# Optimization experiments

Hardware: AMD Instinct MI355X
Metric: run time of the kernel (lower is better)

The kernel has to match this reference:

```python
import jax, jax.numpy as jnp
import numpy as np

NINP, NHID, NPROJ, NLAYER = 240, 1024, 512, 3


def setup_inputs() -> dict:
    key = jax.random.key(0)
    keys = jax.random.split(key, 1 + NLAYER * 6)
    inp = {"x": jax.random.normal(keys[0], (500, 32, NINP), dtype=jnp.float32)}
    kit = iter(keys[1:])
    for l in range(NLAYER):
        nin = NINP if l == 0 else NPROJ
        s = 1.0 / np.sqrt(nin + NPROJ)
        inp[f"W{l}"] = jax.random.uniform(next(kit), (4 * NHID, nin + NPROJ), minval=-s, maxval=s, dtype=jnp.float32)
        inp[f"b{l}"] = jax.random.uniform(next(kit), (4 * NHID,), minval=-s, maxval=s, dtype=jnp.float32)
        sp = 1.0 / np.sqrt(NHID)
        inp[f"P{l}"] = jax.random.uniform(next(kit), (NPROJ, NHID), minval=-sp, maxval=sp, dtype=jnp.float32)
        inp[f"pi{l}"] = jax.random.normal(next(kit), (NHID,), dtype=jnp.float32) * 0.1
        inp[f"pf{l}"] = jax.random.normal(next(kit), (NHID,), dtype=jnp.float32) * 0.1
        inp[f"po{l}"] = jax.random.normal(next(kit), (NHID,), dtype=jnp.float32) * 0.1
    return inp


def _lstmp_layer(x, W, b, P, pi, pf, po):
    # x: [T, B, nin]; returns [T, B, nproj]
    T, B, _ = x.shape
    h0 = jnp.zeros((B, NPROJ), x.dtype)
    c0 = jnp.zeros((B, NHID), x.dtype)

    def step(carry, xt):
        hx, cx = carry
        gates = jnp.concatenate([xt, hx], axis=1) @ W.T + b  # [B, 4*nhid]
        c_in, i_g, f_g, o_g = jnp.split(gates, 4, axis=1)
        i_g = jax.nn.sigmoid(i_g + pi * cx)
        f_g = jax.nn.sigmoid(f_g + pf * cx)
        cy = jnp.clip(f_g * cx + i_g * jnp.tanh(c_in), -50.0, 50.0)
        o_g = jax.nn.sigmoid(o_g + po * cy)
        hy = (o_g * jnp.tanh(cy)) @ P.T  # [B, nproj]
        return (hy, cy), hy

    _, ys = jax.lax.scan(step, (h0, c0), x)
    return ys


def reference(x, W0, b0, P0, pi0, pf0, po0, W1, b1, P1, pi1, pf1, po1, W2, b2, P2, pi2, pf2, po2):
    y = _lstmp_layer(x, W0, b0, P0, pi0, pf0, po0)
    y = _lstmp_layer(y, W1, b1, P1, pi1, pf1, po1)
    y = _lstmp_layer(y, W2, b2, P2, pi2, pf2, po2)
    return y
```

## Files before the change

### kernel.cpp

```cpp
#include <hip/hip_runtime.h>


typedef short s16x4 __attribute__((ext_vector_type(4)));
typedef short s16x8 __attribute__((ext_vector_type(8)));
typedef float f32x4 __attribute__((ext_vector_type(4)));

#define MFMA16(a,b,c) __builtin_amdgcn_mfma_f32_16x16x32_bf16((a),(b),(c),0,0,0)

__device__ __forceinline__ unsigned short f2bf(float f) {
  unsigned int u = __builtin_bit_cast(unsigned int, f);
  u += 0x7FFFu + ((u >> 16) & 1u);
  return (unsigned short)(u >> 16);
}
__device__ __forceinline__ float bf2f(unsigned short h) {
  unsigned int u = ((unsigned int)h) << 16;
  return __builtin_bit_cast(float, u);
}
__device__ __forceinline__ float fsig(float x)  { return __fdividef(1.0f, 1.0f + __expf(-x)); }
__device__ __forceinline__ float ftanh(float x) { return 1.0f - __fdividef(2.0f, 1.0f + __expf(2.0f * x)); }

__device__ __forceinline__ s16x8 cload(const unsigned short* p) {
  unsigned long long a = __hip_atomic_load((unsigned long long*)p,       __ATOMIC_RELAXED, __HIP_MEMORY_SCOPE_AGENT);
  unsigned long long b = __hip_atomic_load((unsigned long long*)(p + 4), __ATOMIC_RELAXED, __HIP_MEMORY_SCOPE_AGENT);
  s16x4 x = __builtin_bit_cast(s16x4, a);
  s16x4 y = __builtin_bit_cast(s16x4, b);
  s16x8 r = {x[0], x[1], x[2], x[3], y[0], y[1], y[2], y[3]};
  return r;
}
__device__ __forceinline__ void cstore1(unsigned short* p, unsigned short v) {
  __hip_atomic_store(p, v, __ATOMIC_RELAXED, __HIP_MEMORY_SCOPE_AGENT);
}

__device__ __forceinline__ void gbar(unsigned int* bar, unsigned int* rel, unsigned int seq) {
  __syncthreads();
  asm volatile("" ::: "memory");
  if (blockIdx.x == 0) {
    const int tid = threadIdx.x;
    if (tid > 0 && tid < 192) {
      while (__hip_atomic_load(&bar[tid * 16], __ATOMIC_RELAXED, __HIP_MEMORY_SCOPE_AGENT) != seq) {
        __builtin_amdgcn_s_sleep(1);
      }
    }
    __syncthreads();
    if (tid == 0) {
      __hip_atomic_store(rel, seq, __ATOMIC_RELAXED, __HIP_MEMORY_SCOPE_AGENT);
    }
  } else {
    if (threadIdx.x == 0) {
      __hip_atomic_store(&bar[blockIdx.x * 16], seq, __ATOMIC_RELAXED, __HIP_MEMORY_SCOPE_AGENT);
      while (__hip_atomic_load(rel, __ATOMIC_RELAXED, __HIP_MEMORY_SCOPE_AGENT) != seq) {
        __builtin_amdgcn_s_sleep(1);
      }
    }
    __syncthreads();
  }
  asm volatile("" ::: "memory");
}

__global__ __launch_bounds__(512, 2) void lstmp_persist(
    const float* __restrict__ x,
    const float* __restrict__ W0, const float* __restrict__ b0, const float* __restrict__ P0,
    const float* __restrict__ pi0, const float* __restrict__ pf0, const float* __restrict__ po0,
    const float* __restrict__ W1, const float* __restrict__ b1, const float* __restrict__ P1,
    const float* __restrict__ pi1, const float* __restrict__ pf1, const float* __restrict__ po1,
    const float* __restrict__ W2, const float* __restrict__ b2, const float* __restrict__ P2,
    const float* __restrict__ pi2, const float* __restrict__ pf2, const float* __restrict__ po2,
    float* __restrict__ out, unsigned char* __restrict__ ws)
{
  const int tid  = threadIdx.x;
  const int bid  = blockIdx.x;
  const int lane = tid & 63;
  const int wv   = tid >> 6;
  const int quad8 = (lane >> 4) * 8;
  const int nrow  = lane & 15;

  unsigned int* bar   = (unsigned int*)ws;
  unsigned int* rel   = bar + 4096;
  unsigned int* mflag = rel + 16;
  unsigned short* xhi = (unsigned short*)(ws + 20480);
  unsigned short* xlo  = xhi  + 4096000;
  unsigned short* hhi  = xlo  + 4096000;
  unsigned short* hlo  = hhi  + 98304;
  unsigned short* mhi  = hlo  + 98304;
  unsigned short* mlo  = mhi  + 98304;

  const float* Wsrc[3] = {W0, W1, W2};
  const float* Psrc[3] = {P0, P1, P2};
  const float* Bsrc[3] = {b0, b1, b2};
  const float* PIs[3]  = {pi0, pi1, pi2};
  const float* PFs[3]  = {pf0, pf1, pf2};
  const float* POs[3]  = {po0, po1, po2};

  __shared__ float exch[8][4][512];
  __shared__ float c_lds[512];
  __shared__ float lds_pad[4096];
  ((volatile float*)lds_pad)[tid & 4095] = 0.0f;

  const unsigned int NT = 192u * 512u;
  const unsigned int gtid = (unsigned int)bid * 512u + (unsigned int)tid;

  const int lA  = bid >> 6;
  const int utA = bid & 63;
  const int ptC = (bid & 63) >> 1;
  const int mtC = bid & 1;

  const int nkbinA  = (lA == 0) ? 8   : 16;
  const int kinpadA = (lA == 0) ? 256 : 512;
  const int kbwA    = (lA == 0) ? 3   : 4;
  const int kwA     = (lA == 0) ? 752 : 1024;
  const int ninA    = (lA == 0) ? 240 : 512;
  const int kb0     = wv * kbwA;

  for (unsigned int i = gtid; i < 4096000u; i += NT) {
    unsigned int k = i & 255u, tb = i >> 8;
    float v = (k < 240u) ? x[tb * 240u + k] : 0.0f;
    unsigned short h = f2bf(v);
    xhi[i] = h; xlo[i] = f2bf(v - bf2f(h));
  }
  for (unsigned int i = gtid; i < 98304u; i += NT) { hhi[i] = 0; hlo[i] = 0; }
  c_lds[tid] = 0.0f;

  s16x8 wgh[4][4], wgl[4][4];
  {
    const float* Wl = Wsrc[lA];
    #pragma unroll
    for (int j = 0; j < 4; ++j) {
      if (j < kbwA) {
        const int kbase = (kb0 + j) * 32 + quad8;
        #pragma unroll
        for (int g = 0; g < 4; ++g) {
          const size_t r = (size_t)((g * 64 + utA) * 16 + nrow);
          #pragma unroll
          for (int jj = 0; jj < 8; ++jj) {
            const int k = kbase + jj;
            float v;
            if (k < kinpadA) v = (lA == 0 && k >= 240) ? 0.0f : Wl[r * kwA + k];
            else             v = Wl[r * kwA + (k - kinpadA + ninA)];
            unsigned short h = f2bf(v);
            wgh[j][g][jj] = (short)h;
            wgl[j][g][jj] = (short)f2bf(v - bf2f(h));
          }
        }
      } else {
        #pragma unroll
        for (int g = 0; g < 4; ++g) { wgh[j][g] = (s16x8)0; wgl[j][g] = (s16x8)0; }
      }
    }
  }
  s16x8 wph[4], wpl[4];
  {
    const float* Pl = Psrc[lA];
    const size_t prow = (size_t)(ptC * 16 + nrow);
    #pragma unroll
    for (int j = 0; j < 4; ++j) {
      const int kbase = (wv * 4 + j) * 32 + quad8;
      #pragma unroll
      for (int jj = 0; jj < 8; ++jj) {
        float v = Pl[prow * 1024u + (size_t)(kbase + jj)];
        unsigned short h = f2bf(v);
        wph[j][jj] = (short)h;
        wpl[j][jj] = (short)f2bf(v - bf2f(h));
      }
    }
  }
  const int uc = utA * 16 + (tid & 15);
  const float rbc = Bsrc[lA][uc];
  const float rbi = Bsrc[lA][1024 + uc];
  const float rbf = Bsrc[lA][2048 + uc];
  const float rbo = Bsrc[lA][3072 + uc];
  const float rpi = PIs[lA][uc];
  const float rpf = PFs[lA][uc];
  const float rpo = POs[lA][uc];

  unsigned int seq = 1;
  __builtin_amdgcn_fence(__ATOMIC_RELEASE, "agent");
  gbar(bar, rel, seq++);
  __builtin_amdgcn_fence(__ATOMIC_ACQUIRE, "agent");

  for (int s = 0; s < 502; ++s) {
    const int t = s - lA;
    const bool act = (t >= 0) && (t < 500);
    const int rbuf = (s + 1) & 1;
    const int wbuf = s & 1;

    if (act) {
      f32x4 acc[4][2];
      #pragma unroll
      for (int g = 0; g < 4; ++g) { acc[g][0] = {0.f,0.f,0.f,0.f}; acc[g][1] = {0.f,0.f,0.f,0.f}; }

      const unsigned short* hbh = hhi + rbuf * 49152;
      const unsigned short* hbl = hlo + rbuf * 49152;

      #pragma unroll
      for (int j = 0; j < 4; ++j) {
        if (j < kbwA) {
          const int kb = kb0 + j;
          s16x8 fa0h, fa0l, fa1h, fa1l;
          if (kb < nkbinA) {
            if (lA == 0) {
              const unsigned short* ph = xhi + (size_t)(t * 32 + nrow) * 256 + kb * 32 + quad8;
              const unsigned short* pl = xlo + (size_t)(t * 32 + nrow) * 256 + kb * 32 + quad8;
              fa0h = *(const s16x8*)ph; fa1h = *(const s16x8*)(ph + 16 * 256);
              fa0l = *(const s16x8*)pl; fa1l = *(const s16x8*)(pl + 16 * 256);
            } else {
              const unsigned short* ph = hbh + (size_t)((lA - 1) * 32 + nrow) * 512 + kb * 32 + quad8;
              const unsigned short* pl = hbl + (size_t)((lA - 1) * 32 + nrow) * 512 + kb * 32 + quad8;
              fa0h = cload(ph); fa1h = cload(ph + 16 * 512);
              fa0l = cload(pl); fa1l = cload(pl + 16 * 512);
            }
          } else {
            const int ko = kb * 32 + quad8 - kinpadA;
            const unsigned short* ph = hbh + (size_t)(lA * 32 + nrow) * 512 + ko;
            const unsigned short* pl = hbl + (size_t)(lA * 32 + nrow) * 512 + ko;
            fa0h = cload(ph); fa1h = cload(ph + 16 * 512);
            fa0l = cload(pl); fa1l = cload(pl + 16 * 512);
          }
          #pragma unroll
          for (int g = 0; g < 4; ++g) {
            acc[g][0] = MFMA16(fa0h, wgh[j][g], acc[g][0]);
            acc[g][0] = MFMA16(fa0l, wgh[j][g], acc[g][0]);
            acc[g][0] = MFMA16(fa0h, wgl[j][g], acc[g][0]);
            acc[g][1] = MFMA16(fa1h, wgh[j][g], acc[g][1]);
            acc[g][1] = MFMA16(fa1l, wgh[j][g], acc[g][1]);
            acc[g][1] = MFMA16(fa1h, wgl[j][g], acc[g][1]);
          }
        }
      }
      #pragma unroll
      for (int g = 0; g < 4; ++g) {
        #pragma unroll
        for (int r = 0; r < 4; ++r) {
          const int m0 = (lane >> 4) * 4 + r;
          exch[wv][g][m0 * 16 + (lane & 15)]        = acc[g][0][r];
          exch[wv][g][(m0 + 16) * 16 + (lane & 15)] = acc[g][1][r];
        }
      }
      __syncthreads();

      {
        const int e = tid, b = tid >> 4;
        float sc = 0.f, si = 0.f, sf = 0.f, so = 0.f;
        #pragma unroll
        for (int w = 0; w < 8; ++w) {
          sc += exch[w][0][e]; si += exch[w][1][e];
          sf += exch[w][2][e]; so += exch[w][3][e];
        }
        const float cin = sc + rbc;
        const float gi  = si + rbi;
        const float gf  = sf + rbf;
        const float go  = so + rbo;
        const float cx  = c_lds[e];
        const float ig  = fsig(gi + rpi * cx);
        const float fg  = fsig(gf + rpf * cx);
        float cy = fg * cx + ig * ftanh(cin);
        cy = fminf(50.0f, fmaxf(-50.0f, cy));
        const float og = fsig(go + rpo * cy);
        const float mv = og * ftanh(cy);
        c_lds[e] = cy;
        const unsigned short mh = f2bf(mv);
        const size_t mi = (size_t)(lA * 32 + b) * 1024 + uc;
        cstore1(mhi + mi, mh);
        cstore1(mlo + mi, f2bf(mv - bf2f(mh)));
      }
      __syncthreads();
      if (tid == 0) {
        __hip_atomic_store(&mflag[lA * 64 + utA], (unsigned int)(s + 1),
                           __ATOMIC_RELAXED, __HIP_MEMORY_SCOPE_AGENT);
      }

      if (wv == 0) {
        const unsigned int want = (unsigned int)(s + 1);
        const unsigned int* fp = mflag + lA * 64 + lane;
        while (__hip_atomic_load(fp, __ATOMIC_RELAXED, __HIP_MEMORY_SCOPE_AGENT) != want) {
          __builtin_amdgcn_s_sleep(1);
        }
      }
      __syncthreads();

      const unsigned short* mah = mhi + (size_t)(lA * 32 + mtC * 16 + nrow) * 1024;
      const unsigned short* mal = mlo + (size_t)(lA * 32 + mtC * 16 + nrow) * 1024;
      f32x4 pacc = {0.f, 0.f, 0.f, 0.f};
      #pragma unroll
      for (int j = 0; j < 4; ++j) {
        const int ko = (wv * 4 + j) * 32 + quad8;
        s16x8 fah = cload(mah + ko);
        s16x8 fal = cload(mal + ko);
        pacc = MFMA16(fah, wph[j], pacc);
        pacc = MFMA16(fal, wph[j], pacc);
        pacc = MFMA16(fah, wpl[j], pacc);
      }
      #pragma unroll
      for (int r = 0; r < 4; ++r) {
        exch[wv][0][((lane >> 4) * 4 + r) * 16 + (lane & 15)] = pacc[r];
      }
      __syncthreads();
      if (tid < 256) {
        float v = 0.f;
        #pragma unroll
        for (int w = 0; w < 8; ++w) v += exch[w][0][tid];
        const int b = mtC * 16 + (tid >> 4);
        const int p = ptC * 16 + (tid & 15);
        const size_t hidx = (size_t)wbuf * 49152 + (size_t)(lA * 32 + b) * 512 + p;
        const unsigned short hh = f2bf(v);
        cstore1(hhi + hidx, hh);
        cstore1(hlo + hidx, f2bf(v - bf2f(hh)));
        if (lA == 2) out[((size_t)t * 32 + b) * 512 + p] = v;
      }
    }
    gbar(bar, rel, seq++);
  }
}

extern "C" void kernel_launch(void* const* d_in, const int* in_sizes, int n_in,
                              void* d_out, int out_size, void* d_ws, size_t ws_size,
                              hipStream_t stream) {
  const float* x   = (const float*)d_in[0];
  const float* W0  = (const float*)d_in[1];
  const float* b0  = (const float*)d_in[2];
  const float* P0  = (const float*)d_in[3];
  const float* pi0 = (const float*)d_in[4];
  const float* pf0 = (const float*)d_in[5];
  const float* po0 = (const float*)d_in[6];
  const float* W1  = (const float*)d_in[7];
  const float* b1  = (const float*)d_in[8];
  const float* P1  = (const float*)d_in[9];
  const float* pi1 = (const float*)d_in[10];
  const float* pf1 = (const float*)d_in[11];
  const float* po1 = (const float*)d_in[12];
  const float* P2_ = nullptr; (void)P2_;
  const float* W2  = (const float*)d_in[13];
  const float* b2  = (const float*)d_in[14];
  const float* P2  = (const float*)d_in[15];
  const float* pi2 = (const float*)d_in[16];
  const float* pf2 = (const float*)d_in[17];
  const float* po2 = (const float*)d_in[18];

  hipLaunchKernelGGL(lstmp_persist, dim3(192), dim3(512), 0, stream,
                     x, W0, b0, P0, pi0, pf0, po0,
                     W1, b1, P1, pi1, pf1, po1,
                     W2, b2, P2, pi2, pf2, po2,
                     (float*)d_out, (unsigned char*)d_ws);
}
```

Measured before the change: 10.01 ms.

## Replace per-step grid barrier with per-layer dataflow flags and 4-deep h buffers

Drops the global grid barrier that ran every wavefront step. Each layer now spins on per-block flags for its own previous h and the lower layer's current h, so the three layers can run decoupled instead of in a lockstep skewed wavefront. The h buffers grow from two to four slots so a faster lower layer can run a few steps ahead, with a back-pressure wait on the upper layer's progress. This removes the cost of the all-block barrier and the idle pipeline fill/drain steps, but adds more flag polling and relies on relaxed atomics plus fences for correct ordering.

```diff
diff --git a/kernel.cpp b/kernel.cpp
--- a/kernel.cpp
+++ b/kernel.cpp
@@ -77,11 +77,12 @@
   unsigned int* bar   = (unsigned int*)ws;
   unsigned int* rel   = bar + 4096;
   unsigned int* mflag = rel + 16;
+  unsigned int* hflag = mflag + 192;
   unsigned short* xhi = (unsigned short*)(ws + 20480);
   unsigned short* xlo  = xhi  + 4096000;
   unsigned short* hhi  = xlo  + 4096000;
-  unsigned short* hlo  = hhi  + 98304;
-  unsigned short* mhi  = hlo  + 98304;
+  unsigned short* hlo  = hhi  + 196608;
+  unsigned short* mhi  = hlo  + 196608;
   unsigned short* mlo  = mhi  + 98304;
 
   const float* Wsrc[3] = {W0, W1, W2};
@@ -117,7 +118,8 @@
     unsigned short h = f2bf(v);
     xhi[i] = h; xlo[i] = f2bf(v - bf2f(h));
   }
-  for (unsigned int i = gtid; i < 98304u; i += NT) { hhi[i] = 0; hlo[i] = 0; }
+  for (unsigned int i = gtid; i < 196608u; i += NT) { hhi[i] = 0; hlo[i] = 0; }
+  if (gtid < 384u) mflag[gtid] = 0u;
   c_lds[tid] = 0.0f;
 
   s16x8 wgh[4][4], wgl[4][4];
@@ -172,142 +174,161 @@
   const float rpf = PFs[lA][uc];
   const float rpo = POs[lA][uc];
 
-  unsigned int seq = 1;
   __builtin_amdgcn_fence(__ATOMIC_RELEASE, "agent");
-  gbar(bar, rel, seq++);
+  gbar(bar, rel, 1u);
   __builtin_amdgcn_fence(__ATOMIC_ACQUIRE, "agent");
 
-  for (int s = 0; s < 502; ++s) {
-    const int t = s - lA;
-    const bool act = (t >= 0) && (t < 500);
-    const int rbuf = (s + 1) & 1;
-    const int wbuf = s & 1;
-
-    if (act) {
-      f32x4 acc[4][2];
-      #pragma unroll
-      for (int g = 0; g < 4; ++g) { acc[g][0] = {0.f,0.f,0.f,0.f}; acc[g][1] = {0.f,0.f,0.f,0.f}; }
-
-      const unsigned short* hbh = hhi + rbuf * 49152;
-      const unsigned short* hbl = hlo + rbuf * 49152;
-
-      #pragma unroll
-      for (int j = 0; j < 4; ++j) {
-        if (j < kbwA) {
-          const int kb = kb0 + j;
-          s16x8 fa0h, fa0l, fa1h, fa1l;
-          if (kb < nkbinA) {
-            if (lA == 0) {
-              const unsigned short* ph = xhi + (size_t)(t * 32 + nrow) * 256 + kb * 32 + quad8;
-              const unsigned short* pl = xlo + (size_t)(t * 32 + nrow) * 256 + kb * 32 + quad8;
-              fa0h = *(const s16x8*)ph; fa1h = *(const s16x8*)(ph + 16 * 256);
-              fa0l = *(const s16x8*)pl; fa1l = *(const s16x8*)(pl + 16 * 256);
-            } else {
-              const unsigned short* ph = hbh + (size_t)((lA - 1) * 32 + nrow) * 512 + kb * 32 + quad8;
-              const unsigned short* pl = hbl + (size_t)((lA - 1) * 32 + nrow) * 512 + kb * 32 + quad8;
-              fa0h = cload(ph); fa1h = cload(ph + 16 * 512);
-              fa0l = cload(pl); fa1l = cload(pl + 16 * 512);
-            }
+  for (int t = 0; t < 500; ++t) {
+    if (wv == 0) {
+      const unsigned int want = (unsigned int)t;
+      const unsigned int* fp = hflag + lA * 64 + lane;
+      while (__hip_atomic_load(fp, __ATOMIC_RELAXED, __HIP_MEMORY_SCOPE_AGENT) < want) {
+        __builtin_amdgcn_s_sleep(1);
+      }
+    } else if (wv == 1 && lA > 0) {
+      const unsigned int want = (unsigned int)(t + 1);
+      const unsigned int* fp = hflag + (lA - 1) * 64 + lane;
+      while (__hip_atomic_load(fp, __ATOMIC_RELAXED, __HIP_MEMORY_SCOPE_AGENT) < want) {
+        __builtin_amdgcn_s_sleep(1);
+      }
+    }
+    __syncthreads();
+
+    const unsigned short* hRecH = hhi + (size_t)(((t + 3) & 3) * 49152 + lA * 16384);
+    const unsigned short* hRecL = hlo + (size_t)(((t + 3) & 3) * 49152 + lA * 16384);
+    const unsigned short* hInH  = hhi + (size_t)((t & 3) * 49152 + (lA - 1) * 16384);
+    const unsigned short* hInL  = hlo + (size_t)((t & 3) * 49152 + (lA - 1) * 16384);
+
+    f32x4 acc[4][2];
+    #pragma unroll
+    for (int g = 0; g < 4; ++g) { acc[g][0] = {0.f,0.f,0.f,0.f}; acc[g][1] = {0.f,0.f,0.f,0.f}; }
+
+    #pragma unroll
+    for (int j = 0; j < 4; ++j) {
+      if (j < kbwA) {
+        const int kb = kb0 + j;
+        s16x8 fa0h, fa0l, fa1h, fa1l;
+        if (kb < nkbinA) {
+          if (lA == 0) {
+            const unsigned short* ph = xhi + (size_t)(t * 32 + nrow) * 256 + kb * 32 + quad8;
+            const unsigned short* pl = xlo + (size_t)(t * 32 + nrow) * 256 + kb * 32 + quad8;
+            fa0h = *(const s16x8*)ph; fa1h = *(const s16x8*)(ph + 16 * 256);
+            fa0l = *(const s16x8*)pl; fa1l = *(const s16x8*)(pl + 16 * 256);
           } else {
-            const int ko = kb * 32 + quad8 - kinpadA;
-            const unsigned short* ph = hbh + (size_t)(lA * 32 + nrow) * 512 + ko;
-            const unsigned short* pl = hbl + (size_t)(lA * 32 + nrow) * 512 + ko;
+            const unsigned short* ph = hInH + (size_t)nrow * 512 + kb * 32 + quad8;
+            const unsigned short* pl = hInL + (size_t)nrow * 512 + kb * 32 + quad8;
             fa0h = cload(ph); fa1h = cload(ph + 16 * 512);
             fa0l = cload(pl); fa1l = cload(pl + 16 * 512);
           }
-          #pragma unroll
-          for (int g = 0; g < 4; ++g) {
-            acc[g][0] = MFMA16(fa0h, wgh[j][g], acc[g][0]);
-            acc[g][0] = MFMA16(fa0l, wgh[j][g], acc[g][0]);
-            acc[g][0] = MFMA16(fa0h, wgl[j][g], acc[g][0]);
-            acc[g][1] = MFMA16(fa1h, wgh[j][g], acc[g][1]);
-            acc[g][1] = MFMA16(fa1l, wgh[j][g], acc[g][1]);
-            acc[g][1] = MFMA16(fa1h, wgl[j][g], acc[g][1]);
-          }
+        } else {
+          const int ko = kb * 32 + quad8 - kinpadA;
+          const unsigned short* ph = hRecH + (size_t)nrow * 512 + ko;
+          const unsigned short* pl = hRecL + (size_t)nrow * 512 + ko;
+          fa0h = cload(ph); fa1h = cload(ph + 16 * 512);
+          fa0l = cload(pl); fa1l = cload(pl + 16 * 512);
         }
-      }
-      #pragma unroll
-      for (int g = 0; g < 4; ++g) {
         #pragma unroll
-        for (int r = 0; r < 4; ++r) {
-          const int m0 = (lane >> 4) * 4 + r;
-          exch[wv][g][m0 * 16 + (lane & 15)]        = acc[g][0][r];
-          exch[wv][g][(m0 + 16) * 16 + (lane & 15)] = acc[g][1][r];
+        for (int g = 0; g < 4; ++g) {
+          acc[g][0] = MFMA16(fa0h, wgh[j][g], acc[g][0]);
+          acc[g][0] = MFMA16(fa0l, wgh[j][g], acc[g][0]);
+          acc[g][0] = MFMA16(fa0h, wgl[j][g], acc[g][0]);
+          acc[g][1] = MFMA16(fa1h, wgh[j][g], acc[g][1]);
+          acc[g][1] = MFMA16(fa1l, wgh[j][g], acc[g][1]);
+          acc[g][1] = MFMA16(fa1h, wgl[j][g], acc[g][1]);
         }
       }
-      __syncthreads();
-
-      {
-        const int e = tid, b = tid >> 4;
-        float sc = 0.f, si = 0.f, sf = 0.f, so = 0.f;
-        #pragma unroll
-        for (int w = 0; w < 8; ++w) {
-          sc += exch[w][0][e]; si += exch[w][1][e];
-          sf += exch[w][2][e]; so += exch[w][3][e];
-        }
-        const float cin = sc + rbc;
-        const float gi  = si + rbi;
-        const float gf  = sf + rbf;
-        const float go  = so + rbo;
-        const float cx  = c_lds[e];
-        const float ig  = fsig(gi + rpi * cx);
-        const float fg  = fsig(gf + rpf * cx);
-        float cy = fg * cx + ig * ftanh(cin);
-        cy = fminf(50.0f, fmaxf(-50.0f, cy));
-        const float og = fsig(go + rpo * cy);
-        const float mv = og * ftanh(cy);
-        c_lds[e] = cy;
-        const unsigned short mh = f2bf(mv);
-        const size_t mi = (size_t)(lA * 32 + b) * 1024 + uc;
-        cstore1(mhi + mi, mh);
-        cstore1(mlo + mi, f2bf(mv - bf2f(mh)));
-      }
-      __syncthreads();
-      if (tid == 0) {
-        __hip_atomic_store(&mflag[lA * 64 + utA], (unsigned int)(s + 1),
-                           __ATOMIC_RELAXED, __HIP_MEMORY_SCOPE_AGENT);
-      }
-
-      if (wv == 0) {
-        const unsigned int want = (unsigned int)(s + 1);
-        const unsigned int* fp = mflag + lA * 64 + lane;
-        while (__hip_atomic_load(fp, __ATOMIC_RELAXED, __HIP_MEMORY_SCOPE_AGENT) != want) {
-          __builtin_amdgcn_s_sleep(1);
-        }
-      }
-      __syncthreads();
-
-      const unsigned short* mah = mhi + (size_t)(lA * 32 + mtC * 16 + nrow) * 1024;
-      const unsigned short* mal = mlo + (size_t)(lA * 32 + mtC * 16 + nrow) * 1024;
-      f32x4 pacc = {0.f, 0.f, 0.f, 0.f};
-      #pragma unroll
-      for (int j = 0; j < 4; ++j) {
-        const int ko = (wv * 4 + j) * 32 + quad8;
-        s16x8 fah = cload(mah + ko);
-        s16x8 fal = cload(mal + ko);
-        pacc = MFMA16(fah, wph[j], pacc);
-        pacc = MFMA16(fal, wph[j], pacc);
-        pacc = MFMA16(fah, wpl[j], pacc);
-      }
+    }
+    #pragma unroll
+    for (int g = 0; g < 4; ++g) {
       #pragma unroll
       for (int r = 0; r < 4; ++r) {
-        exch[wv][0][((lane >> 4) * 4 + r) * 16 + (lane & 15)] = pacc[r];
-      }
-      __syncthreads();
-      if (tid < 256) {
-        float v = 0.f;
-        #pragma unroll
-        for (int w = 0; w < 8; ++w) v += exch[w][0][tid];
-        const int b = mtC * 16 + (tid >> 4);
-        const int p = ptC * 16 + (tid & 15);
-        const size_t hidx = (size_t)wbuf * 49152 + (size_t)(lA * 32 + b) * 512 + p;
-        const unsigned short hh = f2bf(v);
-        cstore1(hhi + hidx, hh);
-        cstore1(hlo + hidx, f2bf(v - bf2f(hh)));
-        if (lA == 2) out[((size_t)t * 32 + b) * 512 + p] = v;
-      }
-    }
-    gbar(bar, rel, seq++);
+        const int m0 = (lane >> 4) * 4 + r;
+        exch[wv][g][m0 * 16 + (lane & 15)]        = acc[g][0][r];
+        exch[wv][g][(m0 + 16) * 16 + (lane & 15)] = acc[g][1][r];
+      }
+    }
+    __syncthreads();
+
+    {
+      const int e = tid, b = tid >> 4;
+      float sc = 0.f, si = 0.f, sf = 0.f, so = 0.f;
+      #pragma unroll
+      for (int w = 0; w < 8; ++w) {
+        sc += exch[w][0][e]; si += exch[w][1][e];
+        sf += exch[w][2][e]; so += exch[w][3][e];
+      }
+      const float cin = sc + rbc;
+      const float gi  = si + rbi;
+      const float gf  = sf + rbf;
+      const float go  = so + rbo;
+      const float cx  = c_lds[e];
+      const float ig  = fsig(gi + rpi * cx);
+      const float fg  = fsig(gf + rpf * cx);
+      float cy = fg * cx + ig * ftanh(cin);
+      cy = fminf(50.0f, fmaxf(-50.0f, cy));
+      const float og = fsig(go + rpo * cy);
+      const float mv = og * ftanh(cy);
+      c_lds[e] = cy;
+      const unsigned short mh = f2bf(mv);
+      const size_t mi = (size_t)(lA * 32 + b) * 1024 + uc;
+      cstore1(mhi + mi, mh);
+      cstore1(mlo + mi, f2bf(mv - bf2f(mh)));
+    }
+    __syncthreads();
+    if (tid == 0) {
+      __hip_atomic_store(&mflag[lA * 64 + utA], (unsigned int)(t + 1),
+                         __ATOMIC_RELAXED, __HIP_MEMORY_SCOPE_AGENT);
+    }
+
+    if (wv == 0) {
+      const unsigned int want = (unsigned int)(t + 1);
+      const unsigned int* fp = mflag + lA * 64 + lane;
+      while (__hip_atomic_load(fp, __ATOMIC_RELAXED, __HIP_MEMORY_SCOPE_AGENT) < want) {
+        __builtin_amdgcn_s_sleep(1);
+      }
+    } else if (wv == 1 && lA < 2 && t >= 4) {
+      const unsigned int want = (unsigned int)(t - 3);
+      const unsigned int* fp = mflag + (lA + 1) * 64 + lane;
+      while (__hip_atomic_load(fp, __ATOMIC_RELAXED, __HIP_MEMORY_SCOPE_AGENT) < want) {
+        __builtin_amdgcn_s_sleep(1);
+      }
+    }
+    __syncthreads();
+
+    const unsigned short* mah = mhi + (size_t)(lA * 32 + mtC * 16 + nrow) * 1024;
+    const unsigned short* mal = mlo + (size_t)(lA * 32 + mtC * 16 + nrow) * 1024;
+    f32x4 pacc = {0.f, 0.f, 0.f, 0.f};
+    #pragma unroll
+    for (int j = 0; j < 4; ++j) {
+      const int ko = (wv * 4 + j) * 32 + quad8;
+      s16x8 fah = cload(mah + ko);
+      s16x8 fal = cload(mal + ko);
+      pacc = MFMA16(fah, wph[j], pacc);
+      pacc = MFMA16(fal, wph[j], pacc);
+      pacc = MFMA16(fah, wpl[j], pacc);
+    }
+    #pragma unroll
+    for (int r = 0; r < 4; ++r) {
+      exch[wv][0][((lane >> 4) * 4 + r) * 16 + (lane & 15)] = pacc[r];
+    }
+    __syncthreads();
+    if (tid < 256) {
+      float v = 0.f;
+      #pragma unroll
+      for (int w = 0; w < 8; ++w) v += exch[w][0][tid];
+      const int b = mtC * 16 + (tid >> 4);
+      const int p = ptC * 16 + (tid & 15);
+      const size_t hidx = (size_t)((t & 3) * 49152 + lA * 16384) + (size_t)b * 512 + p;
+      const unsigned short hh = f2bf(v);
+      cstore1(hhi + hidx, hh);
+      cstore1(hlo + hidx, f2bf(v - bf2f(hh)));
+      if (lA == 2) out[((size_t)t * 32 + b) * 512 + p] = v;
+    }
+    __syncthreads();
+    if (tid == 0) {
+      __hip_atomic_store(&hflag[lA * 64 + (bid & 63)], (unsigned int)(t + 1),
+                         __ATOMIC_RELAXED, __HIP_MEMORY_SCOPE_AGENT);
+    }
   }
 }
 
@@ -327,7 +348,6 @@
   const float* pi1 = (const float*)d_in[10];
   const float* pf1 = (const float*)d_in[11];
   const float* po1 = (const float*)d_in[12];
-  const float* P2_ = nullptr; (void)P2_;
   const float* W2  = (const float*)d_in[13];
   const float* b2  = (const float*)d_in[14];
   const float* P2  = (const float*)d_in[15];
```

After: 11.56 ms. +15.6%, slower.
